# Kernel optimization log

Measured on AMD Instinct MI355X. Metric: run time of the kernel, lower is better.

The kernel has to match this reference:

```python
import jax, jax.numpy as jnp
import numpy as np

D_MODEL = 1024
HEADS = 16


def setup_inputs() -> dict:
    key = jax.random.key(0)
    ks = jax.random.split(key, 11)
    B, S, D = 2, 2048, D_MODEL
    scale = 1.0 / np.sqrt(D)
    inp = {
        "q": jax.random.normal(ks[0], (B, S, D), jnp.float32),
        "k": jax.random.normal(ks[1], (B, S, D), jnp.float32),
        "v": jax.random.normal(ks[2], (B, S, D), jnp.float32),
        "w_q": jax.random.normal(ks[3], (D, D), jnp.float32) * scale,
        "b_q": jnp.zeros((D,), jnp.float32),
        "w_k": jax.random.normal(ks[4], (D, D), jnp.float32) * scale,
        "b_k": jnp.zeros((D,), jnp.float32),
        "w_v": jax.random.normal(ks[5], (D, D), jnp.float32) * scale,
        "b_v": jnp.zeros((D,), jnp.float32),
        "w_o": jax.random.normal(ks[6], (D, D), jnp.float32) * scale,
        "b_o": jnp.zeros((D,), jnp.float32),
    }
    return inp


def reference(q, k, v, w_q, b_q, w_k, b_k, w_v, b_v, w_o, b_o):
    B, S, D = q.shape
    H = HEADS
    Dh = D // H

    def split(x):  # [B,S,D] -> [B,H,S,Dh]
        return x.reshape(B, S, H, Dh).transpose(0, 2, 1, 3)

    qh = split(q @ w_q + b_q)
    kh = split(k @ w_k + b_k)
    vh = split(v @ w_v + b_v)

    # scaled dot-product attention: softmax(Q K^T / sqrt(Dh)) V
    scores = jnp.einsum("bhsd,bhtd->bhst", qh, kh) / jnp.sqrt(
        jnp.asarray(Dh, qh.dtype)
    )
    attn = jax.nn.softmax(scores, axis=-1)
    out = jnp.einsum("bhst,bhtd->bhsd", attn, vh)

    concat = out.transpose(0, 2, 1, 3).reshape(B, S, D)
    return concat @ w_o + b_o
```

## Files before the change

kernel.cpp:

```cpp
#include <hip/hip_runtime.h>
#include <hip/hip_bf16.h>
#include <math.h>

using bf16 = __hip_bfloat16;
typedef __bf16 bf16x8v __attribute__((ext_vector_type(8)));
typedef float f32x4v __attribute__((ext_vector_type(4)));

#define AS1 __attribute__((address_space(1)))
#define AS3 __attribute__((address_space(3)))

__device__ __forceinline__ void g2l16(const void* g, void* l) {
  __builtin_amdgcn_global_load_lds((const AS1 void*)g, (AS3 void*)l, 16, 0, 0);
}

__device__ __forceinline__ float fclamp(float v) {
  return fminf(fmaxf(v, -6.0e4f), 6.0e4f);
}

template <int CTRL>
__device__ __forceinline__ float dpp_f(float x) {
  return __int_as_float(
      __builtin_amdgcn_update_dpp(0, __float_as_int(x), CTRL, 0xF, 0xF, true));
}
__device__ __forceinline__ float red_add16(float x) {
  x += dpp_f<0xB1>(x);
  x += dpp_f<0x4E>(x);
  x += dpp_f<0x124>(x);
  x += dpp_f<0x128>(x);
  return x;
}

#define QSCL 0.1803368801111204f

__global__ __launch_bounds__(256) void transpose_cvt4(
    const float* __restrict__ w0, const float* __restrict__ w1,
    const float* __restrict__ w2, const float* __restrict__ w3,
    bf16* __restrict__ o0, bf16* __restrict__ o1,
    bf16* __restrict__ o2, bf16* __restrict__ o3) {
  const float* in = (blockIdx.z == 0) ? w0 : (blockIdx.z == 1) ? w1
                    : (blockIdx.z == 2) ? w2 : w3;
  bf16* out = (blockIdx.z == 0) ? o0 : (blockIdx.z == 1) ? o1
              : (blockIdx.z == 2) ? o2 : o3;
  __shared__ alignas(16) bf16 tile[64][80];
  const int t = threadIdx.x;
  const int bx = blockIdx.x * 64, by = blockIdx.y * 64;
#pragma unroll
  for (int p = 0; p < 4; ++p) {
    int idx = p * 1024 + t * 4;
    int r = idx >> 6, c0 = idx & 63;
    float4 v = *(const float4*)&in[(size_t)(by + r) * 1024 + bx + c0];
    tile[c0 + 0][r] = __float2bfloat16(v.x);
    tile[c0 + 1][r] = __float2bfloat16(v.y);
    tile[c0 + 2][r] = __float2bfloat16(v.z);
    tile[c0 + 3][r] = __float2bfloat16(v.w);
  }
  __syncthreads();
#pragma unroll
  for (int p = 0; p < 2; ++p) {
    int idx = p * 2048 + t * 8;
    int c = idx >> 6, r0 = idx & 63;
    *(uint4*)&out[(size_t)(bx + c) * 1024 + by + r0] = *(const uint4*)&tile[c][r0];
  }
}

__global__ __launch_bounds__(256) void cvt3(
    const float* __restrict__ q, const float* __restrict__ k,
    const float* __restrict__ v, bf16* __restrict__ oq,
    bf16* __restrict__ ok, bf16* __restrict__ ov) {
  const float* in = (blockIdx.y == 0) ? q : (blockIdx.y == 1) ? k : v;
  bf16* out = (blockIdx.y == 0) ? oq : (blockIdx.y == 1) ? ok : ov;
  int i = (blockIdx.x * 256 + threadIdx.x) * 8;
  float4 a = *(const float4*)&in[i];
  float4 b = *(const float4*)&in[i + 4];
  alignas(16) bf16 tmp[8];
  tmp[0] = __float2bfloat16(a.x); tmp[1] = __float2bfloat16(a.y);
  tmp[2] = __float2bfloat16(a.z); tmp[3] = __float2bfloat16(a.w);
  tmp[4] = __float2bfloat16(b.x); tmp[5] = __float2bfloat16(b.y);
  tmp[6] = __float2bfloat16(b.z); tmp[7] = __float2bfloat16(b.w);
  *(uint4*)&out[i] = *(const uint4*)tmp;
}

__device__ __forceinline__ void qkv_store(bf16* C, int z, int m, int n, float v) {
  int b_ = m >> 11, s_ = m & 2047, h_ = n >> 6, d_ = n & 63;
  size_t oidx = (z == 2)
      ? ((size_t)(b_ * 16 + h_) * 64 + d_) * 2048 + s_
      : ((size_t)(b_ * 16 + h_) * 2048 + s_) * 64 + d_;
  C[oidx] = __float2bfloat16(v);
}

__global__ __launch_bounds__(256, 2) void gemm_qkv_bf16(
    const bf16* __restrict__ Aq, const bf16* __restrict__ Ak,
    const bf16* __restrict__ Av,
    const bf16* __restrict__ WtQ, const bf16* __restrict__ WtK,
    const bf16* __restrict__ WtV,
    const float* __restrict__ bq, const float* __restrict__ bk_,
    const float* __restrict__ bv_,
    bf16* __restrict__ Qh, bf16* __restrict__ Kh, bf16* __restrict__ Vt) {
  constexpr int K = 1024;
  const int z = blockIdx.z;
  const bf16* A    = (z == 0) ? Aq : (z == 1) ? Ak : Av;
  const bf16* Bt   = (z == 0) ? WtQ : (z == 1) ? WtK : WtV;
  const float* bias = (z == 0) ? bq : (z == 1) ? bk_ : bv_;
  bf16* C = (z == 0) ? Qh : (z == 1) ? Kh : Vt;

  __shared__ alignas(16) bf16 As[128 * 32];
  __shared__ alignas(16) bf16 Bs[128 * 32];
  const int t = threadIdx.x;
  const int wave = t >> 6, lane = t & 63;
  const int quad = lane >> 4, l16 = lane & 15;
  const int bm = blockIdx.x * 128, bn = blockIdx.y * 128;
  const int wm = (wave & 1) * 64, wn = (wave >> 1) * 64;

  f32x4v acc[4][4] = {};

  for (int k0 = 0; k0 < K; k0 += 32) {
    __syncthreads();
#pragma unroll
    for (int c = 0; c < 2; ++c) {
      int idx = c * 2048 + t * 8;
      int row = idx >> 5, col = idx & 31;
      g2l16(&A[(size_t)(bm + row) * K + k0 + col], &As[c * 2048 + wave * 512]);
      g2l16(&Bt[(size_t)(bn + row) * K + k0 + col], &Bs[c * 2048 + wave * 512]);
    }
    __syncthreads();

    bf16x8v a[4], b[4];
#pragma unroll
    for (int mi = 0; mi < 4; ++mi)
      a[mi] = *(const bf16x8v*)&As[(wm + mi * 16 + l16) * 32 + quad * 8];
#pragma unroll
    for (int ni = 0; ni < 4; ++ni)
      b[ni] = *(const bf16x8v*)&Bs[(wn + ni * 16 + l16) * 32 + quad * 8];
#pragma unroll
    for (int mi = 0; mi < 4; ++mi)
#pragma unroll
      for (int ni = 0; ni < 4; ++ni)
        acc[mi][ni] = __builtin_amdgcn_mfma_f32_16x16x32_bf16(a[mi], b[ni],
                                                              acc[mi][ni], 0, 0, 0);
  }

  const float scl = (z == 0) ? QSCL : 1.0f;
#pragma unroll
  for (int ni = 0; ni < 4; ++ni) {
    int n = bn + wn + ni * 16 + l16;
    float bz = bias[n];
#pragma unroll
    for (int mi = 0; mi < 4; ++mi)
#pragma unroll
      for (int r = 0; r < 4; ++r) {
        int m = bm + wm + mi * 16 + quad * 4 + r;
        qkv_store(C, z, m, n, fclamp(acc[mi][ni][r] + bz) * scl);
      }
  }
}

__global__ __launch_bounds__(256, 2) void gemm_qkv_f32(
    const float* __restrict__ Aq, const float* __restrict__ Ak,
    const float* __restrict__ Av,
    const bf16* __restrict__ WtQ, const bf16* __restrict__ WtK,
    const bf16* __restrict__ WtV,
    const float* __restrict__ bq, const float* __restrict__ bk_,
    const float* __restrict__ bv_,
    bf16* __restrict__ Qh, bf16* __restrict__ Kh, bf16* __restrict__ Vt) {
  constexpr int K = 1024, LDA = 40;
  const int z = blockIdx.z;
  const float* A  = (z == 0) ? Aq : (z == 1) ? Ak : Av;
  const bf16* Bt  = (z == 0) ? WtQ : (z == 1) ? WtK : WtV;
  const float* bias = (z == 0) ? bq : (z == 1) ? bk_ : bv_;
  bf16* C = (z == 0) ? Qh : (z == 1) ? Kh : Vt;

  __shared__ alignas(16) bf16 As[128 * LDA];
  __shared__ alignas(16) bf16 Bs[128 * LDA];
  const int t = threadIdx.x;
  const int wave = t >> 6, lane = t & 63;
  const int quad = lane >> 4, l16 = lane & 15;
  const int bm = blockIdx.x * 128, bn = blockIdx.y * 128;
  const int wm = (wave & 1) * 64, wn = (wave >> 1) * 64;

  f32x4v acc[4][4] = {};

  for (int k0 = 0; k0 < K; k0 += 32) {
    uint4 va[2], vb[2];
#pragma unroll
    for (int c = 0; c < 2; ++c) {
      int idx = c * 2048 + t * 8;
      int row = idx >> 5, col = idx & 31;
      const float* src = &A[(size_t)(bm + row) * K + k0 + col];
      float4 f0 = *(const float4*)src;
      float4 f1 = *(const float4*)(src + 4);
      alignas(16) bf16 tmp[8];
      tmp[0] = __float2bfloat16(f0.x); tmp[1] = __float2bfloat16(f0.y);
      tmp[2] = __float2bfloat16(f0.z); tmp[3] = __float2bfloat16(f0.w);
      tmp[4] = __float2bfloat16(f1.x); tmp[5] = __float2bfloat16(f1.y);
      tmp[6] = __float2bfloat16(f1.z); tmp[7] = __float2bfloat16(f1.w);
      va[c] = *(const uint4*)tmp;
      vb[c] = *(const uint4*)&Bt[(size_t)(bn + row) * K + k0 + col];
    }
    __syncthreads();
#pragma unroll
    for (int c = 0; c < 2; ++c) {
      int idx = c * 2048 + t * 8;
      int row = idx >> 5, col = idx & 31;
      *(uint4*)&As[row * LDA + col] = va[c];
      *(uint4*)&Bs[row * LDA + col] = vb[c];
    }
    __syncthreads();

    bf16x8v a[4], b[4];
#pragma unroll
    for (int mi = 0; mi < 4; ++mi)
      a[mi] = *(const bf16x8v*)&As[(wm + mi * 16 + l16) * LDA + quad * 8];
#pragma unroll
    for (int ni = 0; ni < 4; ++ni)
      b[ni] = *(const bf16x8v*)&Bs[(wn + ni * 16 + l16) * LDA + quad * 8];
#pragma unroll
    for (int mi = 0; mi < 4; ++mi)
#pragma unroll
      for (int ni = 0; ni < 4; ++ni)
        acc[mi][ni] = __builtin_amdgcn_mfma_f32_16x16x32_bf16(a[mi], b[ni],
                                                              acc[mi][ni], 0, 0, 0);
  }

  const float scl = (z == 0) ? QSCL : 1.0f;
#pragma unroll
  for (int ni = 0; ni < 4; ++ni) {
    int n = bn + wn + ni * 16 + l16;
    float bz = bias[n];
#pragma unroll
    for (int mi = 0; mi < 4; ++mi)
#pragma unroll
      for (int r = 0; r < 4; ++r) {
        int m = bm + wm + mi * 16 + quad * 4 + r;
        qkv_store(C, z, m, n, fclamp(acc[mi][ni][r] + bz) * scl);
      }
  }
}

__global__ __launch_bounds__(256, 2) void gemm_out(
    const bf16* __restrict__ A, const bf16* __restrict__ Bt,
    const float* __restrict__ bias, float* __restrict__ C) {
  constexpr int K = 1024, N = 1024;
  __shared__ alignas(16) bf16 As[128 * 32];
  __shared__ alignas(16) bf16 Bs[64 * 32];
  const int t = threadIdx.x;
  const int wave = t >> 6, lane = t & 63;
  const int quad = lane >> 4, l16 = lane & 15;
  const int bm = blockIdx.x * 128, bn = blockIdx.y * 64;
  const int wm = (wave & 1) * 64, wn = (wave >> 1) * 32;

  f32x4v acc[4][2] = {};

  for (int k0 = 0; k0 < K; k0 += 32) {
    __syncthreads();
#pragma unroll
    for (int c = 0; c < 2; ++c) {
      int idx = c * 2048 + t * 8;
      int row = idx >> 5, col = idx & 31;
      g2l16(&A[(size_t)(bm + row) * K + k0 + col], &As[c * 2048 + wave * 512]);
    }
    {
      int idx = t * 8;
      int row = idx >> 5, col = idx & 31;
      g2l16(&Bt[(size_t)(bn + row) * K + k0 + col], &Bs[wave * 512]);
    }
    __syncthreads();

    bf16x8v a[4], b[2];
#pragma unroll
    for (int mi = 0; mi < 4; ++mi)
      a[mi] = *(const bf16x8v*)&As[(wm + mi * 16 + l16) * 32 + quad * 8];
#pragma unroll
    for (int ni = 0; ni < 2; ++ni)
      b[ni] = *(const bf16x8v*)&Bs[(wn + ni * 16 + l16) * 32 + quad * 8];
#pragma unroll
    for (int mi = 0; mi < 4; ++mi)
#pragma unroll
      for (int ni = 0; ni < 2; ++ni)
        acc[mi][ni] = __builtin_amdgcn_mfma_f32_16x16x32_bf16(a[mi], b[ni],
                                                              acc[mi][ni], 0, 0, 0);
  }

#pragma unroll
  for (int ni = 0; ni < 2; ++ni) {
    int n = bn + wn + ni * 16 + l16;
    float bz = bias[n];
#pragma unroll
    for (int mi = 0; mi < 4; ++mi)
#pragma unroll
      for (int r = 0; r < 4; ++r) {
        int m = bm + wm + mi * 16 + quad * 4 + r;
        C[(size_t)m * N + n] = fclamp(acc[mi][ni][r] + bz);
      }
  }
}

__global__ __launch_bounds__(256, 2) void attn(
    const bf16* __restrict__ Qh, const bf16* __restrict__ Kh,
    const bf16* __restrict__ Vt, bf16* __restrict__ Ctx) {
  constexpr int LDPP = 40;
  __shared__ alignas(16) bf16 Qs[64 * 64];
  __shared__ alignas(16) bf16 Ks[64 * 64];
  __shared__ alignas(16) bf16 Vs[64 * 64];
  __shared__ alignas(16) bf16 Ps[4][16 * LDPP];
  const int t = threadIdx.x;
  const int wave = t >> 6, lane = t & 63;
  const int quad = lane >> 4, l16 = lane & 15;
  const int sw = l16 & 7;
  const int qb = blockIdx.x;
  const int bh = blockIdx.y;
  const size_t bh_off = (size_t)bh * 2048 * 64;
  const bf16* Qb = Qh + bh_off;
  const bf16* Kb = Kh + bh_off;
  const bf16* Vb = Vt + bh_off;

  const int srow = t >> 3;
  const int schunk = t & 7;

#pragma unroll
  for (int c = 0; c < 2; ++c) {
    int row = c * 32 + srow;
    int mc = schunk ^ (row & 7);
    g2l16(&Qb[(size_t)(qb * 64 + row) * 64 + mc * 8], &Qs[c * 2048 + wave * 512]);
  }

  float lrow[4] = {0.f, 0.f, 0.f, 0.f};
  f32x4v oacc[4] = {};

  for (int kt = 0; kt < 32; ++kt) {
    __syncthreads();
#pragma unroll
    for (int c = 0; c < 2; ++c) {
      int row = c * 32 + srow;
      int mc = schunk ^ (row & 7);
      g2l16(&Kb[(size_t)(kt * 64 + row) * 64 + mc * 8], &Ks[c * 2048 + wave * 512]);
      g2l16(&Vb[(size_t)row * 2048 + kt * 64 + mc * 8], &Vs[c * 2048 + wave * 512]);
    }
    __syncthreads();

#pragma unroll
    for (int h = 0; h < 2; ++h) {
      f32x4v s[2] = {};
#pragma unroll
      for (int kk = 0; kk < 2; ++kk) {
        bf16x8v aq = *(const bf16x8v*)
            &Qs[(wave * 16 + l16) * 64 + (((kk * 4 + quad) ^ sw) << 3)];
#pragma unroll
        for (int ni = 0; ni < 2; ++ni) {
          bf16x8v bk = *(const bf16x8v*)
              &Ks[(h * 32 + ni * 16 + l16) * 64 + (((kk * 4 + quad) ^ sw) << 3)];
          s[ni] = __builtin_amdgcn_mfma_f32_16x16x32_bf16(aq, bk, s[ni], 0, 0, 0);
        }
      }

#pragma unroll
      for (int r = 0; r < 4; ++r) {
        float rs = 0.f;
#pragma unroll
        for (int ni = 0; ni < 2; ++ni) {
          float p = exp2f(fminf(s[ni][r], 80.f));
          s[ni][r] = p;
          rs += p;
        }
        lrow[r] += red_add16(rs);
      }

#pragma unroll
      for (int ni = 0; ni < 2; ++ni)
#pragma unroll
        for (int r = 0; r < 4; ++r)
          Ps[wave][(quad * 4 + r) * LDPP + ni * 16 + l16] =
              __float2bfloat16(s[ni][r]);

      {
        bf16x8v ap = *(const bf16x8v*)&Ps[wave][l16 * LDPP + quad * 8];
#pragma unroll
        for (int ni = 0; ni < 4; ++ni) {
          bf16x8v bv = *(const bf16x8v*)
              &Vs[(ni * 16 + l16) * 64 + (((h * 4 + quad) ^ sw) << 3)];
          oacc[ni] = __builtin_amdgcn_mfma_f32_16x16x32_bf16(ap, bv, oacc[ni], 0, 0, 0);
        }
      }
    }
  }

  const int b_ = bh >> 4, h_ = bh & 15;
#pragma unroll
  for (int r = 0; r < 4; ++r) {
    int sr = qb * 64 + wave * 16 + quad * 4 + r;
    float inv = 1.0f / fmaxf(lrow[r], 1.0e-20f);
#pragma unroll
    for (int ni = 0; ni < 4; ++ni) {
      int col = h_ * 64 + ni * 16 + l16;
      Ctx[(size_t)(b_ * 2048 + sr) * 1024 + col] =
          __float2bfloat16(fclamp(oacc[ni][r] * inv));
    }
  }
}

extern "C" void kernel_launch(void* const* d_in, const int* in_sizes, int n_in,
                              void* d_out, int out_size, void* d_ws, size_t ws_size,
                              hipStream_t stream) {
  const float* q   = (const float*)d_in[0];
  const float* k   = (const float*)d_in[1];
  const float* v   = (const float*)d_in[2];
  const float* w_q = (const float*)d_in[3];
  const float* b_q = (const float*)d_in[4];
  const float* w_k = (const float*)d_in[5];
  const float* b_k = (const float*)d_in[6];
  const float* w_v = (const float*)d_in[7];
  const float* b_v = (const float*)d_in[8];
  const float* w_o = (const float*)d_in[9];
  const float* b_o = (const float*)d_in[10];
  float* out = (float*)d_out;

  char* ws = (char*)d_ws;
  const size_t MB = (size_t)1024 * 1024;
  bf16* WtQ = (bf16*)(ws + 0 * MB);
  bf16* WtK = (bf16*)(ws + 2 * MB);
  bf16* WtV = (bf16*)(ws + 4 * MB);
  bf16* WtO = (bf16*)(ws + 6 * MB);

  dim3 tb(256);
  transpose_cvt4<<<dim3(16, 16, 4), tb, 0, stream>>>(w_q, w_k, w_v, w_o,
                                                     WtQ, WtK, WtV, WtO);

  const bool big = ws_size >= (size_t)57 * MB;
  if (big) {
    bf16* Qa  = (bf16*)(ws + 8 * MB);
    bf16* Ka  = (bf16*)(ws + 16 * MB);
    bf16* Va  = (bf16*)(ws + 24 * MB);
    bf16* Qh  = (bf16*)(ws + 32 * MB);
    bf16* Kh  = (bf16*)(ws + 40 * MB);
    bf16* Vt  = (bf16*)(ws + 48 * MB);
    bf16* Ctx = Qa;

    cvt3<<<dim3(2048, 3), tb, 0, stream>>>(q, k, v, Qa, Ka, Va);
    gemm_qkv_bf16<<<dim3(32, 8, 3), tb, 0, stream>>>(Qa, Ka, Va, WtQ, WtK, WtV,
                                                     b_q, b_k, b_v, Qh, Kh, Vt);
    attn<<<dim3(32, 32), tb, 0, stream>>>(Qh, Kh, Vt, Ctx);
    gemm_out<<<dim3(32, 16), tb, 0, stream>>>(Ctx, WtO, b_o, out);
  } else {
    bf16* Qh  = (bf16*)(ws + 8 * MB);
    bf16* Kh  = (bf16*)(ws + 16 * MB);
    bf16* Vt  = (bf16*)(ws + 24 * MB);
    bf16* Ctx = (bf16*)(ws + 32 * MB);

    gemm_qkv_f32<<<dim3(32, 8, 3), tb, 0, stream>>>(q, k, v, WtQ, WtK, WtV,
                                                    b_q, b_k, b_v, Qh, Kh, Vt);
    attn<<<dim3(32, 32), tb, 0, stream>>>(Qh, Kh, Vt, Ctx);
    gemm_out<<<dim3(32, 16), tb, 0, stream>>>(Ctx, WtO, b_o, out);
  }
}
```

Baseline: 263.3 us.

## Double-buffer K/V tiles in attention and compute row sums via MFMA

Attention now double-buffers the K/V shared-memory tiles so the global-to-LDS loads for the next tile overlap compute on the current one, with one barrier per tile instead of two. Q fragments are hoisted into registers once, softmax row sums are computed by an extra MFMA against a ones vector instead of DPP reductions, and s_setprio hints plus a raw exp2 builtin are added. The extra LDS use may lower occupancy, and summing the bf16-rounded probabilities changes the normalisation slightly.

```diff
diff --git a/kernel.cpp b/kernel.cpp
--- a/kernel.cpp
+++ b/kernel.cpp
@@ -15,19 +15,6 @@
 
 __device__ __forceinline__ float fclamp(float v) {
   return fminf(fmaxf(v, -6.0e4f), 6.0e4f);
-}
-
-template <int CTRL>
-__device__ __forceinline__ float dpp_f(float x) {
-  return __int_as_float(
-      __builtin_amdgcn_update_dpp(0, __float_as_int(x), CTRL, 0xF, 0xF, true));
-}
-__device__ __forceinline__ float red_add16(float x) {
-  x += dpp_f<0xB1>(x);
-  x += dpp_f<0x4E>(x);
-  x += dpp_f<0x124>(x);
-  x += dpp_f<0x128>(x);
-  return x;
 }
 
 #define QSCL 0.1803368801111204f
@@ -299,8 +286,8 @@
     const bf16* __restrict__ Vt, bf16* __restrict__ Ctx) {
   constexpr int LDPP = 40;
   __shared__ alignas(16) bf16 Qs[64 * 64];
-  __shared__ alignas(16) bf16 Ks[64 * 64];
-  __shared__ alignas(16) bf16 Vs[64 * 64];
+  __shared__ alignas(16) bf16 Ks[2][64 * 64];
+  __shared__ alignas(16) bf16 Vs[2][64 * 64];
   __shared__ alignas(16) bf16 Ps[4][16 * LDPP];
   const int t = threadIdx.x;
   const int wave = t >> 6, lane = t & 63;
@@ -316,78 +303,95 @@
   const int srow = t >> 3;
   const int schunk = t & 7;
 
+  auto stageKV = [&](int kt, int buf) {
+#pragma unroll
+    for (int c = 0; c < 2; ++c) {
+      int row = c * 32 + srow;
+      int mc = schunk ^ (row & 7);
+      g2l16(&Kb[(size_t)(kt * 64 + row) * 64 + mc * 8],
+            &Ks[buf][c * 2048 + wave * 512]);
+      g2l16(&Vb[(size_t)row * 2048 + kt * 64 + mc * 8],
+            &Vs[buf][c * 2048 + wave * 512]);
+    }
+  };
+
 #pragma unroll
   for (int c = 0; c < 2; ++c) {
     int row = c * 32 + srow;
     int mc = schunk ^ (row & 7);
     g2l16(&Qb[(size_t)(qb * 64 + row) * 64 + mc * 8], &Qs[c * 2048 + wave * 512]);
   }
-
-  float lrow[4] = {0.f, 0.f, 0.f, 0.f};
+  stageKV(0, 0);
+  asm volatile("s_waitcnt vmcnt(0)" ::: "memory");
+  __builtin_amdgcn_s_barrier();
+
+  bf16x8v aq[2];
+#pragma unroll
+  for (int kk = 0; kk < 2; ++kk)
+    aq[kk] = *(const bf16x8v*)
+        &Qs[(wave * 16 + l16) * 64 + (((kk * 4 + quad) ^ sw) << 3)];
+
+  bf16x8v vone;
+#pragma unroll
+  for (int i = 0; i < 8; ++i) vone[i] = (__bf16)1.0f;
+
+  f32x4v lsum = {};
   f32x4v oacc[4] = {};
 
-  for (int kt = 0; kt < 32; ++kt) {
-    __syncthreads();
-#pragma unroll
-    for (int c = 0; c < 2; ++c) {
-      int row = c * 32 + srow;
-      int mc = schunk ^ (row & 7);
-      g2l16(&Kb[(size_t)(kt * 64 + row) * 64 + mc * 8], &Ks[c * 2048 + wave * 512]);
-      g2l16(&Vb[(size_t)row * 2048 + kt * 64 + mc * 8], &Vs[c * 2048 + wave * 512]);
-    }
-    __syncthreads();
-
+  auto compute = [&](int buf) {
 #pragma unroll
     for (int h = 0; h < 2; ++h) {
       f32x4v s[2] = {};
-#pragma unroll
-      for (int kk = 0; kk < 2; ++kk) {
-        bf16x8v aq = *(const bf16x8v*)
-            &Qs[(wave * 16 + l16) * 64 + (((kk * 4 + quad) ^ sw) << 3)];
+      __builtin_amdgcn_s_setprio(1);
+#pragma unroll
+      for (int kk = 0; kk < 2; ++kk)
 #pragma unroll
         for (int ni = 0; ni < 2; ++ni) {
           bf16x8v bk = *(const bf16x8v*)
-              &Ks[(h * 32 + ni * 16 + l16) * 64 + (((kk * 4 + quad) ^ sw) << 3)];
-          s[ni] = __builtin_amdgcn_mfma_f32_16x16x32_bf16(aq, bk, s[ni], 0, 0, 0);
+              &Ks[buf][(h * 32 + ni * 16 + l16) * 64 + (((kk * 4 + quad) ^ sw) << 3)];
+          s[ni] = __builtin_amdgcn_mfma_f32_16x16x32_bf16(aq[kk], bk, s[ni],
+                                                          0, 0, 0);
         }
+      __builtin_amdgcn_s_setprio(0);
+
+#pragma unroll
+      for (int ni = 0; ni < 2; ++ni)
+#pragma unroll
+        for (int r = 0; r < 4; ++r) {
+          float p = __builtin_amdgcn_exp2f(fminf(s[ni][r], 80.f));
+          Ps[wave][(quad * 4 + r) * LDPP + ni * 16 + l16] = __float2bfloat16(p);
+        }
+
+      bf16x8v ap = *(const bf16x8v*)&Ps[wave][l16 * LDPP + quad * 8];
+      __builtin_amdgcn_s_setprio(1);
+      lsum = __builtin_amdgcn_mfma_f32_16x16x32_bf16(ap, vone, lsum, 0, 0, 0);
+#pragma unroll
+      for (int ni = 0; ni < 4; ++ni) {
+        bf16x8v bv = *(const bf16x8v*)
+            &Vs[buf][(ni * 16 + l16) * 64 + (((h * 4 + quad) ^ sw) << 3)];
+        oacc[ni] = __builtin_amdgcn_mfma_f32_16x16x32_bf16(ap, bv, oacc[ni],
+                                                           0, 0, 0);
       }
-
-#pragma unroll
-      for (int r = 0; r < 4; ++r) {
-        float rs = 0.f;
-#pragma unroll
-        for (int ni = 0; ni < 2; ++ni) {
-          float p = exp2f(fminf(s[ni][r], 80.f));
-          s[ni][r] = p;
-          rs += p;
-        }
-        lrow[r] += red_add16(rs);
-      }
-
-#pragma unroll
-      for (int ni = 0; ni < 2; ++ni)
-#pragma unroll
-        for (int r = 0; r < 4; ++r)
-          Ps[wave][(quad * 4 + r) * LDPP + ni * 16 + l16] =
-              __float2bfloat16(s[ni][r]);
-
-      {
-        bf16x8v ap = *(const bf16x8v*)&Ps[wave][l16 * LDPP + quad * 8];
-#pragma unroll
-        for (int ni = 0; ni < 4; ++ni) {
-          bf16x8v bv = *(const bf16x8v*)
-              &Vs[(ni * 16 + l16) * 64 + (((h * 4 + quad) ^ sw) << 3)];
-          oacc[ni] = __builtin_amdgcn_mfma_f32_16x16x32_bf16(ap, bv, oacc[ni], 0, 0, 0);
-        }
-      }
-    }
+      __builtin_amdgcn_s_setprio(0);
+    }
+  };
+
+  for (int kt = 0; kt < 32; kt += 2) {
+    stageKV(kt + 1, 1);
+    compute(0);
+    asm volatile("s_waitcnt vmcnt(0)" ::: "memory");
+    __builtin_amdgcn_s_barrier();
+    if (kt + 2 < 32) stageKV(kt + 2, 0);
+    compute(1);
+    asm volatile("s_waitcnt vmcnt(0)" ::: "memory");
+    __builtin_amdgcn_s_barrier();
   }
 
   const int b_ = bh >> 4, h_ = bh & 15;
 #pragma unroll
   for (int r = 0; r < 4; ++r) {
     int sr = qb * 64 + wave * 16 + quad * 4 + r;
-    float inv = 1.0f / fmaxf(lrow[r], 1.0e-20f);
+    float inv = 1.0f / fmaxf(lsum[r], 1.0e-20f);
 #pragma unroll
     for (int ni = 0; ni < 4; ++ni) {
       int col = h_ * 64 + ni * 16 + l16;
```

Measured after the change: 253.5 us. 3.7% less time.
